# Optimization experiments

Measured on AMD Instinct MI355X. Metric: run time of the kernel, lower is better.

Reference implementation:

```python
import jax, jax.numpy as jnp
import numpy as np
import math

N, B, E = 1024, 1, 1024
H = 16
D = E // H
S = 128  # num_samples per row

def setup_inputs() -> dict:
    key = jax.random.key(0)
    ks = jax.random.split(key, 12)
    w = lambda k: jax.random.normal(k, (E, E), jnp.float32) * 0.02
    inp = {
        'query': jax.random.normal(ks[0], (N, B, E), jnp.float32),
        'key':   jax.random.normal(ks[1], (N, B, E), jnp.float32),
        'value': jax.random.normal(ks[2], (N, B, E), jnp.float32),
        'Wq': w(ks[3]), 'bq': jnp.zeros((E,), jnp.float32),
        'Wk': w(ks[4]), 'bk': jnp.zeros((E,), jnp.float32),
        'Wv': w(ks[5]), 'bv': jnp.zeros((E,), jnp.float32),
        'Wo': w(ks[6]), 'bo': jnp.zeros((E,), jnp.float32),
        # per-row sampled column indices, already offset+clamped to [0, N)
        'samples': jax.random.randint(ks[7], (N, S), 0, N, jnp.int32),
    }
    return inp

def reference(query, key, value, Wq, bq, Wk, bk, Wv, bv, Wo, bo, samples):
    n = query.shape[0]
    # projections (torch Linear: x @ W.T + b), split heads -> [B*H, n, D]
    q = (query @ Wq.T + bq).reshape(n, B * H, D).transpose(1, 0, 2)
    k = (key   @ Wk.T + bk).reshape(n, B * H, D).transpose(1, 0, 2)
    v = (value @ Wv.T + bv).reshape(n, B * H, D).transpose(1, 0, 2)
    # emulate per-row unique(): sort, mask duplicates (first occurrence kept)
    cols = jnp.sort(samples, axis=1)                              # [n, S]
    dup = jnp.concatenate([jnp.zeros((n, 1), bool), cols[:, 1:] == cols[:, :-1]], axis=1)
    kg = k[:, cols]                                               # [BH, n, S, D]
    scores = jnp.einsum('hid,hisd->his', q, kg) / jnp.float32(math.sqrt(n))
    scores = jnp.where(dup[None], jnp.float32(-1e30), scores)
    w = jax.nn.softmax(scores, axis=-1)                           # [BH, n, S]
    vg = v[:, cols]                                               # [BH, n, S, D]
    o = jnp.einsum('his,hisd->hid', w, vg)                        # [BH, n, D]
    o = o.transpose(1, 0, 2).reshape(n, B, E)
    return o @ Wo.T + bo
```

## Files before the change

### kernel.cpp

```cpp
#include <hip/hip_runtime.h>
#include <hip/hip_bf16.h>

#define NTOK 1024
#define EMB  1024
#define NH   16
#define HD   64
#define NS   128

typedef unsigned short u16;
typedef unsigned int uint;
typedef __attribute__((ext_vector_type(8))) unsigned short ushort8v;
typedef __attribute__((ext_vector_type(8))) _Float16 half8v;
typedef __attribute__((ext_vector_type(4))) float f32x4;

__device__ __forceinline__ u16 f2h_bits(float f) {
  union { _Float16 h; u16 u; } x; x.h = (_Float16)f; return x.u;
}

__device__ __forceinline__ void gload16(const u16* g, u16* l) {
  __builtin_amdgcn_global_load_lds(
      (const __attribute__((address_space(1))) uint*)g,
      (__attribute__((address_space(3))) uint*)l, 16, 0, 0);
}

__global__ __launch_bounds__(256) void cvt_mask(const float* __restrict__ S0,
                                                const float* __restrict__ S1,
                                                const float* __restrict__ S2,
                                                const float* __restrict__ S3,
                                                const float* __restrict__ S4,
                                                const float* __restrict__ S5,
                                                const float* __restrict__ S6,
                                                const int* __restrict__ samples,
                                                u16* __restrict__ D,
                                                uint* __restrict__ maskg) {
  const int z = blockIdx.y;
  const int t = threadIdx.x;
  if (z == 7) {
    __shared__ uint m[32];
    const int i = blockIdx.x;
    if (t < 32) m[t] = 0u;
    __syncthreads();
    if (t < NS) {
      const int c = samples[(size_t)i * NS + t];
      atomicOr(&m[c >> 5], 1u << (c & 31));
    }
    __syncthreads();
    if (t < 32) maskg[(size_t)i * 32 + t] = m[t];
    return;
  }
  const float* S;
  switch (z) {
    case 0: S = S0; break;
    case 1: S = S1; break;
    case 2: S = S2; break;
    case 3: S = S3; break;
    case 4: S = S4; break;
    case 5: S = S5; break;
    default: S = S6; break;
  }
  const int idx = blockIdx.x * 256 + t;
  const float4 f = ((const float4*)S)[idx];
  ushort4 p;
  p.x = f2h_bits(f.x); p.y = f2h_bits(f.y);
  p.z = f2h_bits(f.z); p.w = f2h_bits(f.w);
  ((ushort4*)(D + ((size_t)z << 20)))[idx] = p;
}

template<bool OUT_F16>
__global__ __launch_bounds__(256) void gemm3(const u16* __restrict__ Ab,
                                             const u16* __restrict__ Bb,
                                             const float* __restrict__ b0,
                                             const float* __restrict__ b1,
                                             const float* __restrict__ b2,
                                             void* __restrict__ Cp) {
  __shared__ u16 buf[2][2][64 * 32];

  const int t = threadIdx.x;
  const int lane = t & 63;
  const int w = t >> 6;
  const int wr = w >> 1, wc = w & 1;
  const int m0 = blockIdx.y * 64;
  const int n0 = blockIdx.x * 64;
  const int z = blockIdx.z;

  const u16* Az = Ab + ((size_t)z << 20);
  const u16* Bz = Bb + ((size_t)z << 20);
  const float* bsel = (z == 0) ? b0 : ((z == 1) ? b1 : b2);

  const int r_abs = w * 16 + (lane >> 2);
  const int schunk = (lane & 3) ^ ((r_abs >> 1) & 3);
  const u16* gA = Az + (size_t)(m0 + r_abs) * 1024 + schunk * 8;
  const u16* gB = Bz + (size_t)(n0 + r_abs) * 1024 + schunk * 8;
  u16* ldsA[2] = { &buf[0][0][(w * 16) * 32], &buf[1][0][(w * 16) * 32] };
  u16* ldsB[2] = { &buf[0][1][(w * 16) * 32], &buf[1][1][(w * 16) * 32] };

  const int fr = lane & 15;
  const int fq = lane >> 4;
  int offA[2], offB[2];
#pragma unroll
  for (int m = 0; m < 2; m++) {
    const int R = wr * 32 + m * 16 + fr;
    offA[m] = R * 32 + (fq ^ ((R >> 1) & 3)) * 8;
  }
#pragma unroll
  for (int n = 0; n < 2; n++) {
    const int R = wc * 32 + n * 16 + fr;
    offB[n] = R * 32 + (fq ^ ((R >> 1) & 3)) * 8;
  }

  f32x4 acc[2][2];
#pragma unroll
  for (int m = 0; m < 2; m++)
#pragma unroll
    for (int n = 0; n < 2; n++) acc[m][n] = (f32x4){0.f, 0.f, 0.f, 0.f};

  gload16(gA, ldsA[0]);
  gload16(gB, ldsB[0]);

  for (int kt = 0; kt < 32; kt++) {
    const int db = kt & 1;
    if (kt < 31) {
      const int k1 = (kt + 1) * 32;
      gload16(gA + k1, ldsA[db ^ 1]);
      gload16(gB + k1, ldsB[db ^ 1]);
      asm volatile("s_waitcnt vmcnt(2)" ::: "memory");
    } else {
      asm volatile("s_waitcnt vmcnt(0)" ::: "memory");
    }
    __builtin_amdgcn_s_barrier();
    __builtin_amdgcn_sched_barrier(0);

    const u16* cA = &buf[db][0][0];
    const u16* cB = &buf[db][1][0];
    half8v a0 = *(const half8v*)&cA[offA[0]];
    half8v a1 = *(const half8v*)&cA[offA[1]];
    half8v bv0 = *(const half8v*)&cB[offB[0]];
    half8v bv1 = *(const half8v*)&cB[offB[1]];
    acc[0][0] = __builtin_amdgcn_mfma_f32_16x16x32_f16(a0, bv0, acc[0][0], 0, 0, 0);
    acc[0][1] = __builtin_amdgcn_mfma_f32_16x16x32_f16(a0, bv1, acc[0][1], 0, 0, 0);
    acc[1][0] = __builtin_amdgcn_mfma_f32_16x16x32_f16(a1, bv0, acc[1][0], 0, 0, 0);
    acc[1][1] = __builtin_amdgcn_mfma_f32_16x16x32_f16(a1, bv1, acc[1][1], 0, 0, 0);

    asm volatile("s_waitcnt lgkmcnt(0)" ::: "memory");
    __builtin_amdgcn_s_barrier();
    __builtin_amdgcn_sched_barrier(0);
  }

  u16*   Cb = (u16*)Cp   + ((size_t)z << 20);
  float* Cf = (float*)Cp + ((size_t)z << 20);

  if (OUT_F16 && z == 2) {
#pragma unroll
    for (int n = 0; n < 2; n++) {
      const int col = n0 + wc * 32 + n * 16 + fr;
      const float bn = bsel[col];
#pragma unroll
      for (int m = 0; m < 2; m++) {
        const int rbase = m0 + wr * 32 + m * 16 + fq * 4;
        ushort4 pk;
        pk.x = f2h_bits(acc[m][n][0] + bn);
        pk.y = f2h_bits(acc[m][n][1] + bn);
        pk.z = f2h_bits(acc[m][n][2] + bn);
        pk.w = f2h_bits(acc[m][n][3] + bn);
        *(ushort4*)&Cb[(size_t)col * 1024 + rbase] = pk;
      }
    }
    return;
  }

#pragma unroll
  for (int n = 0; n < 2; n++) {
    const int col = n0 + wc * 32 + n * 16 + fr;
    const float bn = bsel[col];
#pragma unroll
    for (int m = 0; m < 2; m++) {
      const int rbase = m0 + wr * 32 + m * 16 + fq * 4;
#pragma unroll
      for (int r = 0; r < 4; r++) {
        const float val = acc[m][n][r] + bn;
        if constexpr (OUT_F16)
          Cb[(size_t)(rbase + r) * 1024 + col] = f2h_bits(val);
        else
          Cf[(size_t)(rbase + r) * 1024 + col] = val;
      }
    }
  }
}

__global__ __launch_bounds__(256) void attn11(const u16* __restrict__ Qh,
                                              const u16* __restrict__ Kh,
                                              const u16* __restrict__ Vtg,
                                              const uint* __restrict__ maskg,
                                              u16* __restrict__ O) {
  const int h  = blockIdx.x;
  const int qt = blockIdx.y;
  const int t  = threadIdx.x;
  const int wid = t >> 6;
  const int lane = t & 63;
  const int fr = lane & 15, fq = lane >> 4;

  __shared__ u16 Kl[3][128 * 64];
  __shared__ u16 Vl[3][64 * 128];
  __shared__ u16 Ps[4][16][136];
  __shared__ uint Ms[64][32];

  {
    const uint4* src = (const uint4*)(maskg + (size_t)qt * 64 * 32);
    uint4* dst = (uint4*)Ms;
    dst[t * 2]     = src[t * 2];
    dst[t * 2 + 1] = src[t * 2 + 1];
  }

  half8v qa0, qa1;
  {
    const u16* qp = Qh + (size_t)(qt * 64 + wid * 16 + fr) * EMB + h * HD + fq * 8;
    qa0 = *(const half8v*)qp;
    qa1 = *(const half8v*)(qp + 32);
  }

  const int kRow = wid * 32 + (lane >> 3);
  const int kChO = ((lane & 7) ^ ((lane >> 3) & 7)) * 8;
  const u16* kBase = Kh + h * HD + kChO;
  const int vSub = lane >> 4;
  const int vCh  = lane & 15;
  const u16* vBase = Vtg + (size_t)h * HD * NTOK;

  auto STAGE = [&](int kt_, int b_) {
#pragma unroll
    for (int ii = 0; ii < 4; ii++) {
      const int row = kRow + ii * 8;
      gload16(kBase + (size_t)(kt_ * 128 + row) * EMB,
              &Kl[b_][(wid * 32 + ii * 8) * 64]);
    }
#pragma unroll
    for (int ii = 0; ii < 4; ii++) {
      const int d = wid * 16 + ii * 4 + vSub;
      const int ch = (vCh ^ (d & 15)) * 8;
      gload16(vBase + (size_t)d * NTOK + kt_ * 128 + ch,
              &Vl[b_][(wid * 16 + ii * 4) * 128]);
    }
  };

  f32x4 oacc[4];
#pragma unroll
  for (int ds = 0; ds < 4; ds++) oacc[ds] = (f32x4){0.f, 0.f, 0.f, 0.f};
  float lsum[4] = {0.f, 0.f, 0.f, 0.f};

  STAGE(0, 0);
  STAGE(1, 1);

#pragma unroll
  for (int kt = 0; kt < 8; kt++) {
    const int cb = kt % 3;
    if (kt < 7) {
      asm volatile("s_waitcnt vmcnt(8) lgkmcnt(0)" ::: "memory");
    } else {
      asm volatile("s_waitcnt vmcnt(0) lgkmcnt(0)" ::: "memory");
    }
    __builtin_amdgcn_s_barrier();
    __builtin_amdgcn_sched_barrier(0);
    if (kt < 6) STAGE(kt + 2, (kt + 2) % 3);

    const u16* Kc = &Kl[cb][0];
    const u16* Vc = &Vl[cb][0];

    uint4 mq[4];
#pragma unroll
    for (int r = 0; r < 4; r++)
      mq[r] = *(const uint4*)&Ms[wid * 16 + fq * 4 + r][kt * 4];

#pragma unroll
    for (int jb = 0; jb < 8; jb++) {
      f32x4 s = (f32x4){0.f, 0.f, 0.f, 0.f};
      const int R = jb * 16 + fr;
      const half8v b0 = *(const half8v*)&Kc[R * 64 + (fq ^ (fr & 7)) * 8];
      const half8v b1 = *(const half8v*)&Kc[R * 64 + ((4 + fq) ^ (fr & 7)) * 8];
      s = __builtin_amdgcn_mfma_f32_16x16x32_f16(qa0, b0, s, 0, 0, 0);
      s = __builtin_amdgcn_mfma_f32_16x16x32_f16(qa1, b1, s, 0, 0, 0);
#pragma unroll
      for (int r = 0; r < 4; r++) {
        const uint mw = (jb >> 1) == 0 ? mq[r].x
                      : (jb >> 1) == 1 ? mq[r].y
                      : (jb >> 1) == 2 ? mq[r].z : mq[r].w;
        const float p = ((mw >> ((jb & 1) * 16 + fr)) & 1u)
                            ? __expf(s[r] * 0.03125f) : 0.f;
        lsum[r] += p;
        Ps[wid][fq * 4 + r][jb * 16 + fr] = f2h_bits(p);
      }
    }
    asm volatile("s_waitcnt lgkmcnt(0)" ::: "memory");
    __builtin_amdgcn_sched_barrier(0);

    __builtin_amdgcn_s_setprio(1);
#pragma unroll
    for (int jc = 0; jc < 4; jc++) {
      const half8v pa = *(const half8v*)&Ps[wid][fr][jc * 32 + fq * 8];
#pragma unroll
      for (int ds = 0; ds < 4; ds++) {
        const int d = ds * 16 + fr;
        const half8v vb = *(const half8v*)&Vc[d * 128 + ((jc * 4 + fq) ^ fr) * 8];
        oacc[ds] = __builtin_amdgcn_mfma_f32_16x16x32_f16(pa, vb, oacc[ds], 0, 0, 0);
      }
    }
    __builtin_amdgcn_s_setprio(0);
  }

#pragma unroll
  for (int r = 0; r < 4; r++) {
    float v = lsum[r];
#pragma unroll
    for (int off = 1; off < 16; off <<= 1) v += __shfl_xor(v, off, 16);
    lsum[r] = v;
  }

#pragma unroll
  for (int ds = 0; ds < 4; ds++) {
#pragma unroll
    for (int r = 0; r < 4; r++) {
      O[(size_t)(qt * 64 + wid * 16 + fq * 4 + r) * EMB + h * HD + ds * 16 + fr] =
          f2h_bits(oacc[ds][r] / lsum[r]);
    }
  }
}

extern "C" void kernel_launch(void* const* d_in, const int* in_sizes, int n_in,
                              void* d_out, int out_size, void* d_ws, size_t ws_size,
                              hipStream_t stream) {
  const float* query = (const float*)d_in[0];
  const float* key   = (const float*)d_in[1];
  const float* value = (const float*)d_in[2];
  const float* Wq    = (const float*)d_in[3];
  const float* bq    = (const float*)d_in[4];
  const float* Wk    = (const float*)d_in[5];
  const float* bk    = (const float*)d_in[6];
  const float* Wv    = (const float*)d_in[7];
  const float* bv    = (const float*)d_in[8];
  const float* Wo    = (const float*)d_in[9];
  const float* bo    = (const float*)d_in[10];
  const int* samples = (const int*)d_in[11];
  float* out = (float*)d_out;

  u16* base = (u16*)d_ws;
  u16* Xh = base;
  u16* Wh = base + ((size_t)3 << 20);
  u16* Qh = base + ((size_t)7 << 20);
  u16* Kh = base + ((size_t)8 << 20);
  u16* Vt = base + ((size_t)9 << 20);
  u16* O  = base + ((size_t)10 << 20);
  uint* maskg = (uint*)(base + ((size_t)11 << 20));

  cvt_mask<<<dim3(1024, 8), 256, 0, stream>>>(
      query, key, value, Wq, Wk, Wv, Wo, samples, Xh, maskg);

  gemm3<true><<<dim3(16, 16, 3), 256, 0, stream>>>(Xh, Wh, bq, bk, bv, Qh);

  attn11<<<dim3(NH, 16), 256, 0, stream>>>(Qh, Kh, Vt, maskg, O);

  gemm3<false><<<dim3(16, 16, 1), 256, 0, stream>>>(O, Wh + ((size_t)3 << 20), bo, bo, bo, out);
}
```

Before: 59.83 us.

## Fuse fp32-to-fp16 conversion into GEMM loads and build sample mask inside attention

Removes the separate conversion/mask kernel. The GEMMs now read fp32 activations and weights directly, convert them in registers and store fp16 tiles to LDS. The attention kernel builds its per-row sample bitmask from the raw sample indices with LDS atomics. This saves one launch and the fp16 intermediate round-trip through global memory. In exchange, each GEMM block re-converts the fp32 tiles it reads, moves twice as many bytes per tile, and replaces async global-to-LDS loads with register staging behind a full vmcnt wait, which may expose more load latency.

```diff
diff --git a/kernel.cpp b/kernel.cpp
--- a/kernel.cpp
+++ b/kernel.cpp
@@ -23,57 +23,23 @@
       (__attribute__((address_space(3))) uint*)l, 16, 0, 0);
 }
 
-__global__ __launch_bounds__(256) void cvt_mask(const float* __restrict__ S0,
-                                                const float* __restrict__ S1,
-                                                const float* __restrict__ S2,
-                                                const float* __restrict__ S3,
-                                                const float* __restrict__ S4,
-                                                const float* __restrict__ S5,
-                                                const float* __restrict__ S6,
-                                                const int* __restrict__ samples,
-                                                u16* __restrict__ D,
-                                                uint* __restrict__ maskg) {
-  const int z = blockIdx.y;
-  const int t = threadIdx.x;
-  if (z == 7) {
-    __shared__ uint m[32];
-    const int i = blockIdx.x;
-    if (t < 32) m[t] = 0u;
-    __syncthreads();
-    if (t < NS) {
-      const int c = samples[(size_t)i * NS + t];
-      atomicOr(&m[c >> 5], 1u << (c & 31));
-    }
-    __syncthreads();
-    if (t < 32) maskg[(size_t)i * 32 + t] = m[t];
-    return;
-  }
-  const float* S;
-  switch (z) {
-    case 0: S = S0; break;
-    case 1: S = S1; break;
-    case 2: S = S2; break;
-    case 3: S = S3; break;
-    case 4: S = S4; break;
-    case 5: S = S5; break;
-    default: S = S6; break;
-  }
-  const int idx = blockIdx.x * 256 + t;
-  const float4 f = ((const float4*)S)[idx];
-  ushort4 p;
-  p.x = f2h_bits(f.x); p.y = f2h_bits(f.y);
-  p.z = f2h_bits(f.z); p.w = f2h_bits(f.w);
-  ((ushort4*)(D + ((size_t)z << 20)))[idx] = p;
-}
-
-template<bool OUT_F16>
-__global__ __launch_bounds__(256) void gemm3(const u16* __restrict__ Ab,
-                                             const u16* __restrict__ Bb,
-                                             const float* __restrict__ b0,
-                                             const float* __restrict__ b1,
-                                             const float* __restrict__ b2,
-                                             void* __restrict__ Cp) {
-  __shared__ u16 buf[2][2][64 * 32];
+__device__ __forceinline__ ushort8v cvt8(const float4 x0, const float4 x1) {
+  ushort8v p;
+  p[0] = f2h_bits(x0.x); p[1] = f2h_bits(x0.y);
+  p[2] = f2h_bits(x0.z); p[3] = f2h_bits(x0.w);
+  p[4] = f2h_bits(x1.x); p[5] = f2h_bits(x1.y);
+  p[6] = f2h_bits(x1.z); p[7] = f2h_bits(x1.w);
+  return p;
+}
+
+template<bool A_F16, bool OUT_F16>
+__global__ __launch_bounds__(256) void gemm4(
+    const void* __restrict__ A0, const void* __restrict__ A1, const void* __restrict__ A2,
+    const float* __restrict__ B0, const float* __restrict__ B1, const float* __restrict__ B2,
+    const float* __restrict__ b0, const float* __restrict__ b1, const float* __restrict__ b2,
+    void* __restrict__ Cp) {
+  __shared__ u16 As[2][64 * 32];
+  __shared__ u16 Bs[2][64 * 32];
 
   const int t = threadIdx.x;
   const int lane = t & 63;
@@ -83,16 +49,19 @@
   const int n0 = blockIdx.x * 64;
   const int z = blockIdx.z;
 
-  const u16* Az = Ab + ((size_t)z << 20);
-  const u16* Bz = Bb + ((size_t)z << 20);
+  const void*  Asel = (z == 0) ? A0 : ((z == 1) ? A1 : A2);
+  const float* Bsel = (z == 0) ? B0 : ((z == 1) ? B1 : B2);
   const float* bsel = (z == 0) ? b0 : ((z == 1) ? b1 : b2);
 
+  const int srow = t >> 2;
+  const int scC  = t & 3;
+  const int dcW  = scC ^ ((srow >> 1) & 3);
+
+  const float* gB = Bsel + (size_t)(n0 + srow) * 1024 + scC * 8;
+  const float* gAf = (const float*)Asel + (size_t)(m0 + srow) * 1024 + scC * 8;
   const int r_abs = w * 16 + (lane >> 2);
   const int schunk = (lane & 3) ^ ((r_abs >> 1) & 3);
-  const u16* gA = Az + (size_t)(m0 + r_abs) * 1024 + schunk * 8;
-  const u16* gB = Bz + (size_t)(n0 + r_abs) * 1024 + schunk * 8;
-  u16* ldsA[2] = { &buf[0][0][(w * 16) * 32], &buf[1][0][(w * 16) * 32] };
-  u16* ldsB[2] = { &buf[0][1][(w * 16) * 32], &buf[1][1][(w * 16) * 32] };
+  const u16* gAh = (const u16*)Asel + (size_t)(m0 + r_abs) * 1024 + schunk * 8;
 
   const int fr = lane & 15;
   const int fq = lane >> 4;
@@ -114,36 +83,54 @@
 #pragma unroll
     for (int n = 0; n < 2; n++) acc[m][n] = (f32x4){0.f, 0.f, 0.f, 0.f};
 
-  gload16(gA, ldsA[0]);
-  gload16(gB, ldsB[0]);
+  if constexpr (A_F16) {
+    gload16(gAh, &As[0][(w * 16) * 32]);
+  } else {
+    const float4 a0 = *(const float4*)gAf;
+    const float4 a1 = *(const float4*)(gAf + 4);
+    *(ushort8v*)&As[0][srow * 32 + dcW * 8] = cvt8(a0, a1);
+  }
+  {
+    const float4 x0 = *(const float4*)gB;
+    const float4 x1 = *(const float4*)(gB + 4);
+    *(ushort8v*)&Bs[0][srow * 32 + dcW * 8] = cvt8(x0, x1);
+  }
+  if constexpr (A_F16) asm volatile("s_waitcnt vmcnt(0)" ::: "memory");
 
   for (int kt = 0; kt < 32; kt++) {
     const int db = kt & 1;
+    asm volatile("s_waitcnt lgkmcnt(0)" ::: "memory");
+    __builtin_amdgcn_s_barrier();
+    __builtin_amdgcn_sched_barrier(0);
+
+    float4 a0n, a1n, b0n, b1n;
     if (kt < 31) {
       const int k1 = (kt + 1) * 32;
-      gload16(gA + k1, ldsA[db ^ 1]);
-      gload16(gB + k1, ldsB[db ^ 1]);
-      asm volatile("s_waitcnt vmcnt(2)" ::: "memory");
-    } else {
-      asm volatile("s_waitcnt vmcnt(0)" ::: "memory");
-    }
-    __builtin_amdgcn_s_barrier();
-    __builtin_amdgcn_sched_barrier(0);
-
-    const u16* cA = &buf[db][0][0];
-    const u16* cB = &buf[db][1][0];
-    half8v a0 = *(const half8v*)&cA[offA[0]];
-    half8v a1 = *(const half8v*)&cA[offA[1]];
-    half8v bv0 = *(const half8v*)&cB[offB[0]];
-    half8v bv1 = *(const half8v*)&cB[offB[1]];
+      if constexpr (A_F16) {
+        gload16(gAh + k1, &As[db ^ 1][(w * 16) * 32]);
+      } else {
+        a0n = *(const float4*)(gAf + k1);
+        a1n = *(const float4*)(gAf + k1 + 4);
+      }
+      b0n = *(const float4*)(gB + k1);
+      b1n = *(const float4*)(gB + k1 + 4);
+    }
+
+    half8v a0 = *(const half8v*)&As[db][offA[0]];
+    half8v a1 = *(const half8v*)&As[db][offA[1]];
+    half8v bv0 = *(const half8v*)&Bs[db][offB[0]];
+    half8v bv1 = *(const half8v*)&Bs[db][offB[1]];
     acc[0][0] = __builtin_amdgcn_mfma_f32_16x16x32_f16(a0, bv0, acc[0][0], 0, 0, 0);
     acc[0][1] = __builtin_amdgcn_mfma_f32_16x16x32_f16(a0, bv1, acc[0][1], 0, 0, 0);
     acc[1][0] = __builtin_amdgcn_mfma_f32_16x16x32_f16(a1, bv0, acc[1][0], 0, 0, 0);
     acc[1][1] = __builtin_amdgcn_mfma_f32_16x16x32_f16(a1, bv1, acc[1][1], 0, 0, 0);
 
-    asm volatile("s_waitcnt lgkmcnt(0)" ::: "memory");
-    __builtin_amdgcn_s_barrier();
-    __builtin_amdgcn_sched_barrier(0);
+    if (kt < 31) {
+      asm volatile("s_waitcnt vmcnt(0)" ::: "memory");
+      if constexpr (!A_F16)
+        *(ushort8v*)&As[db ^ 1][srow * 32 + dcW * 8] = cvt8(a0n, a1n);
+      *(ushort8v*)&Bs[db ^ 1][srow * 32 + dcW * 8] = cvt8(b0n, b1n);
+    }
   }
 
   u16*   Cb = (u16*)Cp   + ((size_t)z << 20);
@@ -187,10 +174,10 @@
   }
 }
 
-__global__ __launch_bounds__(256) void attn11(const u16* __restrict__ Qh,
+__global__ __launch_bounds__(256) void attn12(const u16* __restrict__ Qh,
                                               const u16* __restrict__ Kh,
                                               const u16* __restrict__ Vtg,
-                                              const uint* __restrict__ maskg,
+                                              const int* __restrict__ samples,
                                               u16* __restrict__ O) {
   const int h  = blockIdx.x;
   const int qt = blockIdx.y;
@@ -205,10 +192,21 @@
   __shared__ uint Ms[64][32];
 
   {
-    const uint4* src = (const uint4*)(maskg + (size_t)qt * 64 * 32);
-    uint4* dst = (uint4*)Ms;
-    dst[t * 2]     = src[t * 2];
-    dst[t * 2 + 1] = src[t * 2 + 1];
+    uint* msf = (uint*)Ms;
+#pragma unroll
+    for (int j = 0; j < 8; j++) msf[t + j * 256] = 0u;
+    __syncthreads();
+    const int4* sp = (const int4*)(samples + (size_t)(qt * 64) * NS);
+#pragma unroll
+    for (int j = 0; j < 8; j++) {
+      const int i4 = t + j * 256;
+      const int4 c4 = sp[i4];
+      const int row = i4 >> 5;
+      atomicOr(&msf[row * 32 + (c4.x >> 5)], 1u << (c4.x & 31));
+      atomicOr(&msf[row * 32 + (c4.y >> 5)], 1u << (c4.y & 31));
+      atomicOr(&msf[row * 32 + (c4.z >> 5)], 1u << (c4.z & 31));
+      atomicOr(&msf[row * 32 + (c4.w >> 5)], 1u << (c4.w & 31));
+    }
   }
 
   half8v qa0, qa1;
@@ -341,20 +339,16 @@
   float* out = (float*)d_out;
 
   u16* base = (u16*)d_ws;
-  u16* Xh = base;
-  u16* Wh = base + ((size_t)3 << 20);
-  u16* Qh = base + ((size_t)7 << 20);
-  u16* Kh = base + ((size_t)8 << 20);
-  u16* Vt = base + ((size_t)9 << 20);
-  u16* O  = base + ((size_t)10 << 20);
-  uint* maskg = (uint*)(base + ((size_t)11 << 20));
-
-  cvt_mask<<<dim3(1024, 8), 256, 0, stream>>>(
-      query, key, value, Wq, Wk, Wv, Wo, samples, Xh, maskg);
-
-  gemm3<true><<<dim3(16, 16, 3), 256, 0, stream>>>(Xh, Wh, bq, bk, bv, Qh);
-
-  attn11<<<dim3(NH, 16), 256, 0, stream>>>(Qh, Kh, Vt, maskg, O);
-
-  gemm3<false><<<dim3(16, 16, 1), 256, 0, stream>>>(O, Wh + ((size_t)3 << 20), bo, bo, bo, out);
-}
+  u16* Qh = base;
+  u16* Kh = base + ((size_t)1 << 20);
+  u16* Vt = base + ((size_t)2 << 20);
+  u16* O  = base + ((size_t)3 << 20);
+
+  gemm4<false, true><<<dim3(16, 16, 3), 256, 0, stream>>>(
+      query, key, value, Wq, Wk, Wv, bq, bk, bv, Qh);
+
+  attn12<<<dim3(NH, 16), 256, 0, stream>>>(Qh, Kh, Vt, samples, O);
+
+  gemm4<true, false><<<dim3(16, 16, 1), 256, 0, stream>>>(
+      O, O, O, Wo, Wo, Wo, bo, bo, bo, out);
+}
```

Result: slower. 67.55 us (+12.9%).
